# Kernel optimization log

Measured on AMD Instinct MI355X. Metric: run time of the kernel, lower is better.

Reference implementation:

```python
import jax, jax.numpy as jnp
import numpy as np


def setup_inputs() -> dict:
    key = jax.random.key(0)
    k0, k1, k2, k3 = jax.random.split(key, 4)
    B, N, D, C, F = 8192, 784, 64, 10, 2  # batch, input_dim, bond_dim, num_classes, feature_dim
    x = jax.random.uniform(k0, (B, N), dtype=jnp.float32)  # pixel values in [0,1]
    core0 = jax.random.normal(k1, (F, 1, D), dtype=jnp.float32) * 0.1
    base = jnp.broadcast_to(jnp.eye(D, dtype=jnp.float32), (N - 2, F, D, D))
    cores_mid = base + jax.random.normal(k2, (N - 2, F, D, D), dtype=jnp.float32) * 0.01
    core_last = jax.random.normal(k3, (F, D, C), dtype=jnp.float32) * 0.1
    return {"x": x, "core0": core0, "cores_mid": cores_mid, "core_last": core_last}


def reference(x, core0, cores_mid, core_last):
    EPS = 1e-8
    factor = jnp.float32(np.pi / 2.0)
    # FeatureMap: [B, N] -> [B, N, 2] with (cos, sin)
    feats = jnp.stack([jnp.cos(factor * x), jnp.sin(factor * x)], axis=-1)
    # First site: M = v0 @ A0.squeeze(1)  -> [B, D]
    M = jnp.einsum('bf,fd->bd', feats[:, 0, :], core0[:, 0, :])
    # Sequential left->right contraction over middle sites with per-step L2 normalization
    v_mid = jnp.moveaxis(feats[:, 1:-1, :], 1, 0)  # [N-2, B, 2]

    def step(M, inp):
        v, A = inp  # v: [B, 2], A: [2, D, D]
        Mn = jnp.einsum('bi,bf,fij->bj', M, v, A)
        Mn = Mn / (jnp.linalg.norm(Mn, axis=1, keepdims=True) + EPS)
        return Mn, None

    M, _ = jax.lax.scan(step, M, (v_mid, cores_mid))
    # Last site: logits[b,c] = sum_i M[b,i] * (v_N[b,f] A_N[f,i,c])
    logits = jnp.einsum('bi,bf,fic->bc', M, feats[:, -1, :], core_last)
    return logits
```

## Files before the change

kernel.cpp:

```cpp
#include <hip/hip_runtime.h>

typedef __attribute__((ext_vector_type(8))) short s16x8;
typedef __attribute__((ext_vector_type(4))) float f32x4;
typedef __attribute__((ext_vector_type(4))) int i32x4;

#define NMID 782
#define PI_2 1.5707963267948966f
#define EG_STEP_BYTES 16384
#define EG_ELEMS ((size_t)NMID * 8192)
#define XCH_CH 3072
#define XCH_PAR 6144

__device__ __forceinline__ int cvt_pk_bf16(float a, float b) {
  int r;
  asm("v_cvt_pk_bf16_f32 %0, %1, %2" : "=v"(r) : "v"(a), "v"(b));
  return r;
}

__device__ __forceinline__ f32x4 mfma_bf16(i32x4 a, i32x4 b, f32x4 c) {
  return __builtin_amdgcn_mfma_f32_16x16x32_bf16(
      __builtin_bit_cast(s16x8, a), __builtin_bit_cast(s16x8, b), c, 0, 0, 0);
}

__device__ __forceinline__ unsigned short bf16_rne(float v) {
  unsigned u = __float_as_uint(v);
  return (unsigned short)((u + 0x7FFFu + ((u >> 16) & 1)) >> 16);
}

__global__ __launch_bounds__(256) void prep_eg(const float* __restrict__ cm,
                                               unsigned short* __restrict__ eg) {
  const int n = blockIdx.x;
  const float* src = cm + (size_t)n * 8192;
  unsigned short* dst = eg + (size_t)n * 8192;
#pragma unroll
  for (int it = 0; it < 4; ++it) {
    int row = it * 256 + threadIdx.x;
    int q = row >> 6, l = row & 63;
    int t = q >> 2, cc = q & 3;
    int f = cc >> 1, c2 = cc & 1, h = l >> 4;
    int j = 16 * t + (l & 15);
    unsigned short v8[8];
#pragma unroll
    for (int e = 0; e < 8; ++e) {
      int i = 32 * c2 + 16 * (e >> 2) + 4 * h + (e & 3);
      float val = src[(f * 64 + i) * 64 + j] - (i == j ? 1.0f : 0.0f);
      v8[e] = bf16_rne(val);
    }
    *(uint4*)(dst + (size_t)row * 8) = *(const uint4*)v8;
  }
}

#define STEP2G(nc, CUR, NXT, X0v, X1v, RS0, RS1)                            \
  {                                                                         \
    int np = (nc) + 3;                                                      \
    if (np >= NMID) np = NMID - 1;                                          \
    const char* pnxt = base + (size_t)np * EG_STEP_BYTES;                   \
    _Pragma("unroll") for (int q = 0; q < 4; ++q)                           \
        NXT[q] = *(const i32x4*)(pnxt + q * 1024);                          \
    float c0, s0, c1, s1;                                                   \
    __sincosf(PI_2 * (X0v), &s0, &c0);                                      \
    __sincosf(PI_2 * (X1v), &s1, &c1);                                      \
    c0 *= (RS0);                                                            \
    s0 *= (RS0);                                                            \
    c1 *= (RS1);                                                            \
    s1 *= (RS1);                                                            \
    f32x4 z = {0.f, 0.f, 0.f, 0.f};                                         \
    __builtin_amdgcn_s_setprio(1);                                          \
    f32x4 aA0 = mfma_bf16(CUR[0], B0g0, z);                                 \
    aA0 = mfma_bf16(CUR[1], B1g0, aA0);                                     \
    f32x4 aB0 = mfma_bf16(CUR[2], B0g0, z);                                 \
    aB0 = mfma_bf16(CUR[3], B1g0, aB0);                                     \
    f32x4 aA1 = mfma_bf16(CUR[0], B0g1, z);                                 \
    aA1 = mfma_bf16(CUR[1], B1g1, aA1);                                     \
    f32x4 aB1 = mfma_bf16(CUR[2], B0g1, z);                                 \
    aB1 = mfma_bf16(CUR[3], B1g1, aB1);                                     \
    __builtin_amdgcn_s_setprio(0);                                          \
    char* wb = xlds + (((nc) + 1) & 1) * XCH_PAR + h * 768 + bl * 48 +      \
               wv * 8;                                                      \
    float cps0 = c0 + s0;                                                   \
    f32x4 mn0;                                                              \
    _Pragma("unroll") for (int r = 0; r < 4; ++r)                           \
        mn0[r] = cps0 * own0[r] + c0 * aA0[r] + s0 * aB0[r];                \
    own0 = mn0;                                                             \
    int2 w0;                                                                \
    w0.x = cvt_pk_bf16(mn0[0], mn0[1]);                                     \
    w0.y = cvt_pk_bf16(mn0[2], mn0[3]);                                     \
    *(int2*)(wb) = w0;                                                      \
    float cps1 = c1 + s1;                                                   \
    f32x4 mn1;                                                              \
    _Pragma("unroll") for (int r = 0; r < 4; ++r)                           \
        mn1[r] = cps1 * own1[r] + c1 * aA1[r] + s1 * aB1[r];                \
    own1 = mn1;                                                             \
    int2 w1;                                                                \
    w1.x = cvt_pk_bf16(mn1[0], mn1[1]);                                     \
    w1.y = cvt_pk_bf16(mn1[2], mn1[3]);                                     \
    *(int2*)(wb + XCH_CH) = w1;                                             \
    asm volatile("s_waitcnt lgkmcnt(0)" ::: "memory");                      \
    __builtin_amdgcn_s_barrier();                                           \
    __builtin_amdgcn_sched_barrier(0);                                      \
    {                                                                       \
      const char* rb =                                                      \
          xlds + (((nc) + 1) & 1) * XCH_PAR + h * 768 + bl * 48;            \
      B0g0 = *(const i32x4*)(rb);                                           \
      B1g0 = *(const i32x4*)(rb + 16);                                      \
      B0g1 = *(const i32x4*)(rb + XCH_CH);                                  \
      B1g1 = *(const i32x4*)(rb + XCH_CH + 16);                             \
    }                                                                       \
  }

__global__ __launch_bounds__(256, 2) void mps_main(
    const float* __restrict__ x, const float* __restrict__ core0,
    const float* __restrict__ core_last, const unsigned short* __restrict__ eg,
    float* __restrict__ out) {
  __shared__ alignas(16) char xlds[2 * XCH_PAR];
  const int lane = threadIdx.x & 63;
  const int wv = threadIdx.x >> 6;
  const int bl = lane & 15;
  const int h = lane >> 4;
  const int b0 = blockIdx.x * 32 + bl;
  const int b1 = b0 + 16;
  const float* xr0 = x + (size_t)b0 * 784;
  const float* xr1 = x + (size_t)b1 * 784;
  const char* base = (const char*)eg + (size_t)wv * 4096 + (size_t)lane * 16;

  f32x4 own0, own1;
  i32x4 B0g0, B1g0, B0g1, B1g1;
  {
    float s, c;
    __sincosf(PI_2 * xr0[0], &s, &c);
    float fm[16];
#pragma unroll
    for (int t = 0; t < 4; ++t)
#pragma unroll
      for (int r = 0; r < 4; ++r) {
        int j = 16 * t + 4 * h + r;
        fm[t * 4 + r] = c * core0[j] + s * core0[64 + j];
      }
#pragma unroll
    for (int r = 0; r < 4; ++r) own0[r] = fm[wv * 4 + r];
#pragma unroll
    for (int p = 0; p < 4; ++p) {
      B0g0[p] = cvt_pk_bf16(fm[2 * p], fm[2 * p + 1]);
      B1g0[p] = cvt_pk_bf16(fm[8 + 2 * p], fm[8 + 2 * p + 1]);
    }
  }
  {
    float s, c;
    __sincosf(PI_2 * xr1[0], &s, &c);
    float fm[16];
#pragma unroll
    for (int t = 0; t < 4; ++t)
#pragma unroll
      for (int r = 0; r < 4; ++r) {
        int j = 16 * t + 4 * h + r;
        fm[t * 4 + r] = c * core0[j] + s * core0[64 + j];
      }
#pragma unroll
    for (int r = 0; r < 4; ++r) own1[r] = fm[wv * 4 + r];
#pragma unroll
    for (int p = 0; p < 4; ++p) {
      B0g1[p] = cvt_pk_bf16(fm[2 * p], fm[2 * p + 1]);
      B1g1[p] = cvt_pk_bf16(fm[8 + 2 * p], fm[8 + 2 * p + 1]);
    }
  }

  i32x4 frA[4], frB[4], frC[4], frD[4];
#pragma unroll
  for (int q = 0; q < 4; ++q)
    frA[q] = *(const i32x4*)(base + 0 * EG_STEP_BYTES + q * 1024);
#pragma unroll
  for (int q = 0; q < 4; ++q)
    frB[q] = *(const i32x4*)(base + 1 * EG_STEP_BYTES + q * 1024);
#pragma unroll
  for (int q = 0; q < 4; ++q)
    frC[q] = *(const i32x4*)(base + 2 * EG_STEP_BYTES + q * 1024);

  float xq0[12], xq1[12];
  f32x4 xfA0, xfB0, xfA1, xfB1;
  *(f32x4*)&xq0[0] = *(const f32x4*)(xr0 + 0);
  *(f32x4*)&xq0[4] = *(const f32x4*)(xr0 + 4);
  *(f32x4*)&xq0[8] = *(const f32x4*)(xr0 + 8);
  *(f32x4*)&xq1[0] = *(const f32x4*)(xr1 + 0);
  *(f32x4*)&xq1[4] = *(const f32x4*)(xr1 + 4);
  *(f32x4*)&xq1[8] = *(const f32x4*)(xr1 + 8);

  for (int g = 0; g < 97; ++g) {
    if (g > 0) {
#pragma unroll
      for (int i = 0; i < 4; ++i) {
        xq0[i] = xq0[8 + i];
        xq1[i] = xq1[8 + i];
      }
      *(f32x4*)&xq0[4] = xfA0;
      *(f32x4*)&xq0[8] = xfB0;
      *(f32x4*)&xq1[4] = xfA1;
      *(f32x4*)&xq1[8] = xfB1;
    }
    {
      int xo = (g < 96) ? 8 * g + 12 : 780;
      int xo2 = (g < 96) ? 8 * g + 16 : 780;
      xfA0 = *(const f32x4*)(xr0 + xo);
      xfB0 = *(const f32x4*)(xr0 + xo2);
      xfA1 = *(const f32x4*)(xr1 + xo);
      xfB1 = *(const f32x4*)(xr1 + xo2);
    }

    float rs0 = 1.0f, rs1 = 1.0f;
    if ((g & 7) == 0) {
      float ss0 = 0.f, ss1 = 0.f;
#pragma unroll
      for (int p = 0; p < 4; ++p) {
        unsigned u0 = (unsigned)B0g0[p], u1 = (unsigned)B1g0[p];
        float a0 = __uint_as_float(u0 << 16);
        float a1 = __uint_as_float(u0 & 0xFFFF0000u);
        float d0 = __uint_as_float(u1 << 16);
        float d1 = __uint_as_float(u1 & 0xFFFF0000u);
        ss0 += a0 * a0 + a1 * a1 + d0 * d0 + d1 * d1;
        unsigned v0 = (unsigned)B0g1[p], v1 = (unsigned)B1g1[p];
        float e0 = __uint_as_float(v0 << 16);
        float e1 = __uint_as_float(v0 & 0xFFFF0000u);
        float f0 = __uint_as_float(v1 << 16);
        float f1 = __uint_as_float(v1 & 0xFFFF0000u);
        ss1 += e0 * e0 + e1 * e1 + f0 * f0 + f1 * f1;
      }
      ss0 += __shfl_xor(ss0, 16);
      ss0 += __shfl_xor(ss0, 32);
      ss1 += __shfl_xor(ss1, 16);
      ss1 += __shfl_xor(ss1, 32);
      rs0 = rsqrtf(ss0);
      rs1 = rsqrtf(ss1);
    }

    int n0 = 8 * g;
    STEP2G(n0 + 0, frA, frD, xq0[1], xq1[1], rs0, rs1);
    STEP2G(n0 + 1, frB, frA, xq0[2], xq1[2], 1.0f, 1.0f);
    STEP2G(n0 + 2, frC, frB, xq0[3], xq1[3], 1.0f, 1.0f);
    STEP2G(n0 + 3, frD, frC, xq0[4], xq1[4], 1.0f, 1.0f);
    STEP2G(n0 + 4, frA, frD, xq0[5], xq1[5], 1.0f, 1.0f);
    STEP2G(n0 + 5, frB, frA, xq0[6], xq1[6], 1.0f, 1.0f);
    STEP2G(n0 + 6, frC, frB, xq0[7], xq1[7], 1.0f, 1.0f);
    STEP2G(n0 + 7, frD, frC, xq0[8], xq1[8], 1.0f, 1.0f);
  }

  {
#pragma unroll
    for (int i = 0; i < 4; ++i) {
      xq0[i] = xq0[8 + i];
      xq1[i] = xq1[8 + i];
    }
    *(f32x4*)&xq0[4] = xfA0;
    *(f32x4*)&xq1[4] = xfA1;
    STEP2G(776, frA, frD, xq0[1], xq1[1], 1.0f, 1.0f);
    STEP2G(777, frB, frA, xq0[2], xq1[2], 1.0f, 1.0f);
    STEP2G(778, frC, frB, xq0[3], xq1[3], 1.0f, 1.0f);
    STEP2G(779, frD, frC, xq0[4], xq1[4], 1.0f, 1.0f);
    STEP2G(780, frA, frD, xq0[5], xq1[5], 1.0f, 1.0f);
    STEP2G(781, frB, frA, xq0[6], xq1[6], 1.0f, 1.0f);
  }

  asm volatile("s_waitcnt lgkmcnt(0)" ::: "memory");
  __builtin_amdgcn_s_barrier();
  *(f32x4*)(xlds + wv * 1152 + lane * 16) = own0;
  *(f32x4*)(xlds + 4608 + wv * 1152 + lane * 16) = own1;
  asm volatile("s_waitcnt lgkmcnt(0)" ::: "memory");
  __builtin_amdgcn_s_barrier();
  __builtin_amdgcn_sched_barrier(0);

#pragma unroll
  for (int grp = 0; grp < 2; ++grp) {
    float fm[16];
#pragma unroll
    for (int t = 0; t < 4; ++t) {
      f32x4 v = *(const f32x4*)(xlds + grp * 4608 + t * 1152 + lane * 16);
#pragma unroll
      for (int r = 0; r < 4; ++r) fm[t * 4 + r] = v[r];
    }
    float ss = 0.f;
#pragma unroll
    for (int i = 0; i < 16; ++i) ss += fm[i] * fm[i];
    ss += __shfl_xor(ss, 16);
    ss += __shfl_xor(ss, 32);
    float inv = 1.0f / (sqrtf(ss) + 1e-8f);
#pragma unroll
    for (int i = 0; i < 16; ++i) fm[i] *= inv;

    float xv = grp == 0 ? xq0[7] : xq1[7];
    float s, c;
    __sincosf(PI_2 * xv, &s, &c);
    float part[10];
#pragma unroll
    for (int cc = 0; cc < 10; ++cc) part[cc] = 0.f;
#pragma unroll
    for (int t = 0; t < 4; ++t)
#pragma unroll
      for (int r = 0; r < 4; ++r) {
        int i = 16 * t + 4 * h + r;
        float mv = fm[t * 4 + r];
#pragma unroll
        for (int cc = 0; cc < 10; ++cc)
          part[cc] +=
              mv * (c * core_last[i * 10 + cc] + s * core_last[640 + i * 10 + cc]);
      }
#pragma unroll
    for (int cc = 0; cc < 10; ++cc) {
      part[cc] += __shfl_xor(part[cc], 16);
      part[cc] += __shfl_xor(part[cc], 32);
    }
    if (wv == 0 && h == 0) {
      int brow = grp == 0 ? b0 : b1;
#pragma unroll
      for (int cc = 0; cc < 10; ++cc) out[brow * 10 + cc] = part[cc];
    }
  }
}

__global__ __launch_bounds__(64) void mps_slow(const float* __restrict__ x,
                                               const float* __restrict__ core0,
                                               const float* __restrict__ cm,
                                               const float* __restrict__ cl,
                                               float* __restrict__ out) {
  int b = blockIdx.x * 64 + threadIdx.x;
  float m[64], mn[64];
  float s, c;
  __sincosf(PI_2 * x[(size_t)b * 784], &s, &c);
  for (int d = 0; d < 64; ++d) m[d] = c * core0[d] + s * core0[64 + d];
  for (int n = 0; n < NMID; ++n) {
    __sincosf(PI_2 * x[(size_t)b * 784 + n + 1], &s, &c);
    const float* A0 = cm + (size_t)n * 8192;
    const float* A1 = A0 + 4096;
    for (int j = 0; j < 64; ++j) mn[j] = 0.f;
    for (int i = 0; i < 64; ++i) {
      float w0 = c * m[i], w1 = s * m[i];
      for (int j = 0; j < 64; ++j) mn[j] += w0 * A0[i * 64 + j] + w1 * A1[i * 64 + j];
    }
    float ssn = 0.f;
    for (int j = 0; j < 64; ++j) ssn += mn[j] * mn[j];
    float inv = 1.f / (sqrtf(ssn) + 1e-8f);
    for (int j = 0; j < 64; ++j) m[j] = mn[j] * inv;
  }
  __sincosf(PI_2 * x[(size_t)b * 784 + 783], &s, &c);
  for (int cc = 0; cc < 10; ++cc) {
    float acc = 0.f;
    for (int i = 0; i < 64; ++i)
      acc += m[i] * (c * cl[i * 10 + cc] + s * cl[640 + i * 10 + cc]);
    out[b * 10 + cc] = acc;
  }
}

extern "C" void kernel_launch(void* const* d_in, const int* in_sizes, int n_in,
                              void* d_out, int out_size, void* d_ws, size_t ws_size,
                              hipStream_t stream) {
  const float* x = (const float*)d_in[0];
  const float* core0 = (const float*)d_in[1];
  const float* cm = (const float*)d_in[2];
  const float* cl = (const float*)d_in[3];
  float* out = (float*)d_out;
  size_t need = EG_ELEMS * sizeof(unsigned short);
  if (ws_size >= need) {
    unsigned short* eg = (unsigned short*)d_ws;
    prep_eg<<<NMID, 256, 0, stream>>>(cm, eg);
    mps_main<<<256, 256, 0, stream>>>(x, core0, cl, eg, out);
  } else {
    mps_slow<<<8192 / 64, 64, 0, stream>>>(x, core0, cm, cl, out);
  }
}
```

Baseline: 245.9 us.

## Collapse four-wave block into single wave per 32 rows, removing LDS exchange

Each block now uses one 64-lane wavefront that computes all four 16-column output tiles of the 64-wide state itself, instead of splitting them across four waves that exchanged bf16 state through LDS with a barrier every step. This removes the per-step LDS write/read and block barrier. In exchange each wave issues four times the MFMAs per step, holds the whole core slice (16 x 16B fragments, double buffered) in registers with only one step of prefetch, and the grid drops to 256 single-wave blocks, so far fewer waves are available to hide the serial MFMA and load latency.

```diff
diff --git a/kernel.cpp b/kernel.cpp
--- a/kernel.cpp
+++ b/kernel.cpp
@@ -8,8 +8,6 @@
 #define PI_2 1.5707963267948966f
 #define EG_STEP_BYTES 16384
 #define EG_ELEMS ((size_t)NMID * 8192)
-#define XCH_CH 3072
-#define XCH_PAR 6144
 
 __device__ __forceinline__ int cvt_pk_bf16(float a, float b) {
   int r;
@@ -50,12 +48,12 @@
   }
 }
 
-#define STEP2G(nc, CUR, NXT, X0v, X1v, RS0, RS1)                            \
+#define STEP2C(nc, CUR, NXT, X0v, X1v, RS0, RS1)                            \
   {                                                                         \
-    int np = (nc) + 3;                                                      \
+    int np = (nc) + 1;                                                      \
     if (np >= NMID) np = NMID - 1;                                          \
     const char* pnxt = base + (size_t)np * EG_STEP_BYTES;                   \
-    _Pragma("unroll") for (int q = 0; q < 4; ++q)                           \
+    _Pragma("unroll") for (int q = 0; q < 16; ++q)                          \
         NXT[q] = *(const i32x4*)(pnxt + q * 1024);                          \
     float c0, s0, c1, s1;                                                   \
     __sincosf(PI_2 * (X0v), &s0, &c0);                                      \
@@ -64,116 +62,77 @@
     s0 *= (RS0);                                                            \
     c1 *= (RS1);                                                            \
     s1 *= (RS1);                                                            \
+    float cps0 = c0 + s0, cps1 = c1 + s1;                                   \
     f32x4 z = {0.f, 0.f, 0.f, 0.f};                                         \
-    __builtin_amdgcn_s_setprio(1);                                          \
-    f32x4 aA0 = mfma_bf16(CUR[0], B0g0, z);                                 \
-    aA0 = mfma_bf16(CUR[1], B1g0, aA0);                                     \
-    f32x4 aB0 = mfma_bf16(CUR[2], B0g0, z);                                 \
-    aB0 = mfma_bf16(CUR[3], B1g0, aB0);                                     \
-    f32x4 aA1 = mfma_bf16(CUR[0], B0g1, z);                                 \
-    aA1 = mfma_bf16(CUR[1], B1g1, aA1);                                     \
-    f32x4 aB1 = mfma_bf16(CUR[2], B0g1, z);                                 \
-    aB1 = mfma_bf16(CUR[3], B1g1, aB1);                                     \
-    __builtin_amdgcn_s_setprio(0);                                          \
-    char* wb = xlds + (((nc) + 1) & 1) * XCH_PAR + h * 768 + bl * 48 +      \
-               wv * 8;                                                      \
-    float cps0 = c0 + s0;                                                   \
-    f32x4 mn0;                                                              \
-    _Pragma("unroll") for (int r = 0; r < 4; ++r)                           \
-        mn0[r] = cps0 * own0[r] + c0 * aA0[r] + s0 * aB0[r];                \
-    own0 = mn0;                                                             \
-    int2 w0;                                                                \
-    w0.x = cvt_pk_bf16(mn0[0], mn0[1]);                                     \
-    w0.y = cvt_pk_bf16(mn0[2], mn0[3]);                                     \
-    *(int2*)(wb) = w0;                                                      \
-    float cps1 = c1 + s1;                                                   \
-    f32x4 mn1;                                                              \
-    _Pragma("unroll") for (int r = 0; r < 4; ++r)                           \
-        mn1[r] = cps1 * own1[r] + c1 * aA1[r] + s1 * aB1[r];                \
-    own1 = mn1;                                                             \
-    int2 w1;                                                                \
-    w1.x = cvt_pk_bf16(mn1[0], mn1[1]);                                     \
-    w1.y = cvt_pk_bf16(mn1[2], mn1[3]);                                     \
-    *(int2*)(wb + XCH_CH) = w1;                                             \
-    asm volatile("s_waitcnt lgkmcnt(0)" ::: "memory");                      \
-    __builtin_amdgcn_s_barrier();                                           \
-    __builtin_amdgcn_sched_barrier(0);                                      \
-    {                                                                       \
-      const char* rb =                                                      \
-          xlds + (((nc) + 1) & 1) * XCH_PAR + h * 768 + bl * 48;            \
-      B0g0 = *(const i32x4*)(rb);                                           \
-      B1g0 = *(const i32x4*)(rb + 16);                                      \
-      B0g1 = *(const i32x4*)(rb + XCH_CH);                                  \
-      B1g1 = *(const i32x4*)(rb + XCH_CH + 16);                             \
+    _Pragma("unroll") for (int t = 0; t < 4; ++t) {                         \
+      __builtin_amdgcn_s_setprio(1);                                        \
+      f32x4 aA0 = mfma_bf16(CUR[4 * t + 0], B0a, z);                        \
+      aA0 = mfma_bf16(CUR[4 * t + 1], B1a, aA0);                            \
+      f32x4 aB0 = mfma_bf16(CUR[4 * t + 2], B0a, z);                        \
+      aB0 = mfma_bf16(CUR[4 * t + 3], B1a, aB0);                            \
+      f32x4 aA1 = mfma_bf16(CUR[4 * t + 0], B0b, z);                        \
+      aA1 = mfma_bf16(CUR[4 * t + 1], B1b, aA1);                            \
+      f32x4 aB1 = mfma_bf16(CUR[4 * t + 2], B0b, z);                        \
+      aB1 = mfma_bf16(CUR[4 * t + 3], B1b, aB1);                            \
+      __builtin_amdgcn_s_setprio(0);                                        \
+      _Pragma("unroll") for (int r = 0; r < 4; ++r) {                       \
+        m0[4 * t + r] = cps0 * m0[4 * t + r] + c0 * aA0[r] + s0 * aB0[r];   \
+        m1[4 * t + r] = cps1 * m1[4 * t + r] + c1 * aA1[r] + s1 * aB1[r];   \
+      }                                                                     \
     }                                                                       \
-  }
-
-__global__ __launch_bounds__(256, 2) void mps_main(
+    _Pragma("unroll") for (int p = 0; p < 4; ++p) {                         \
+      B0a[p] = cvt_pk_bf16(m0[2 * p], m0[2 * p + 1]);                       \
+      B1a[p] = cvt_pk_bf16(m0[8 + 2 * p], m0[8 + 2 * p + 1]);               \
+      B0b[p] = cvt_pk_bf16(m1[2 * p], m1[2 * p + 1]);                       \
+      B1b[p] = cvt_pk_bf16(m1[8 + 2 * p], m1[8 + 2 * p + 1]);               \
+    }                                                                       \
+  }
+
+__global__ __launch_bounds__(64) void mps_main(
     const float* __restrict__ x, const float* __restrict__ core0,
     const float* __restrict__ core_last, const unsigned short* __restrict__ eg,
     float* __restrict__ out) {
-  __shared__ alignas(16) char xlds[2 * XCH_PAR];
-  const int lane = threadIdx.x & 63;
-  const int wv = threadIdx.x >> 6;
+  const int lane = threadIdx.x;
   const int bl = lane & 15;
   const int h = lane >> 4;
   const int b0 = blockIdx.x * 32 + bl;
   const int b1 = b0 + 16;
   const float* xr0 = x + (size_t)b0 * 784;
   const float* xr1 = x + (size_t)b1 * 784;
-  const char* base = (const char*)eg + (size_t)wv * 4096 + (size_t)lane * 16;
-
-  f32x4 own0, own1;
-  i32x4 B0g0, B1g0, B0g1, B1g1;
+  const char* base = (const char*)eg + (size_t)lane * 16;
+
+  float m0[16], m1[16];
+  i32x4 B0a, B1a, B0b, B1b;
   {
     float s, c;
     __sincosf(PI_2 * xr0[0], &s, &c);
-    float fm[16];
 #pragma unroll
     for (int t = 0; t < 4; ++t)
 #pragma unroll
       for (int r = 0; r < 4; ++r) {
         int j = 16 * t + 4 * h + r;
-        fm[t * 4 + r] = c * core0[j] + s * core0[64 + j];
-      }
-#pragma unroll
-    for (int r = 0; r < 4; ++r) own0[r] = fm[wv * 4 + r];
-#pragma unroll
-    for (int p = 0; p < 4; ++p) {
-      B0g0[p] = cvt_pk_bf16(fm[2 * p], fm[2 * p + 1]);
-      B1g0[p] = cvt_pk_bf16(fm[8 + 2 * p], fm[8 + 2 * p + 1]);
-    }
-  }
-  {
-    float s, c;
+        m0[t * 4 + r] = c * core0[j] + s * core0[64 + j];
+      }
     __sincosf(PI_2 * xr1[0], &s, &c);
-    float fm[16];
 #pragma unroll
     for (int t = 0; t < 4; ++t)
 #pragma unroll
       for (int r = 0; r < 4; ++r) {
         int j = 16 * t + 4 * h + r;
-        fm[t * 4 + r] = c * core0[j] + s * core0[64 + j];
-      }
-#pragma unroll
-    for (int r = 0; r < 4; ++r) own1[r] = fm[wv * 4 + r];
+        m1[t * 4 + r] = c * core0[j] + s * core0[64 + j];
+      }
 #pragma unroll
     for (int p = 0; p < 4; ++p) {
-      B0g1[p] = cvt_pk_bf16(fm[2 * p], fm[2 * p + 1]);
-      B1g1[p] = cvt_pk_bf16(fm[8 + 2 * p], fm[8 + 2 * p + 1]);
-    }
-  }
-
-  i32x4 frA[4], frB[4], frC[4], frD[4];
-#pragma unroll
-  for (int q = 0; q < 4; ++q)
-    frA[q] = *(const i32x4*)(base + 0 * EG_STEP_BYTES + q * 1024);
-#pragma unroll
-  for (int q = 0; q < 4; ++q)
-    frB[q] = *(const i32x4*)(base + 1 * EG_STEP_BYTES + q * 1024);
-#pragma unroll
-  for (int q = 0; q < 4; ++q)
-    frC[q] = *(const i32x4*)(base + 2 * EG_STEP_BYTES + q * 1024);
+      B0a[p] = cvt_pk_bf16(m0[2 * p], m0[2 * p + 1]);
+      B1a[p] = cvt_pk_bf16(m0[8 + 2 * p], m0[8 + 2 * p + 1]);
+      B0b[p] = cvt_pk_bf16(m1[2 * p], m1[2 * p + 1]);
+      B1b[p] = cvt_pk_bf16(m1[8 + 2 * p], m1[8 + 2 * p + 1]);
+    }
+  }
+
+  i32x4 frA[16], frB[16];
+#pragma unroll
+  for (int q = 0; q < 16; ++q) frA[q] = *(const i32x4*)(base + q * 1024);
 
   float xq0[12], xq1[12];
   f32x4 xfA0, xfB0, xfA1, xfB1;
@@ -209,19 +168,9 @@
     if ((g & 7) == 0) {
       float ss0 = 0.f, ss1 = 0.f;
 #pragma unroll
-      for (int p = 0; p < 4; ++p) {
-        unsigned u0 = (unsigned)B0g0[p], u1 = (unsigned)B1g0[p];
-        float a0 = __uint_as_float(u0 << 16);
-        float a1 = __uint_as_float(u0 & 0xFFFF0000u);
-        float d0 = __uint_as_float(u1 << 16);
-        float d1 = __uint_as_float(u1 & 0xFFFF0000u);
-        ss0 += a0 * a0 + a1 * a1 + d0 * d0 + d1 * d1;
-        unsigned v0 = (unsigned)B0g1[p], v1 = (unsigned)B1g1[p];
-        float e0 = __uint_as_float(v0 << 16);
-        float e1 = __uint_as_float(v0 & 0xFFFF0000u);
-        float f0 = __uint_as_float(v1 << 16);
-        float f1 = __uint_as_float(v1 & 0xFFFF0000u);
-        ss1 += e0 * e0 + e1 * e1 + f0 * f0 + f1 * f1;
+      for (int i = 0; i < 16; ++i) {
+        ss0 += m0[i] * m0[i];
+        ss1 += m1[i] * m1[i];
       }
       ss0 += __shfl_xor(ss0, 16);
       ss0 += __shfl_xor(ss0, 32);
@@ -232,14 +181,14 @@
     }
 
     int n0 = 8 * g;
-    STEP2G(n0 + 0, frA, frD, xq0[1], xq1[1], rs0, rs1);
-    STEP2G(n0 + 1, frB, frA, xq0[2], xq1[2], 1.0f, 1.0f);
-    STEP2G(n0 + 2, frC, frB, xq0[3], xq1[3], 1.0f, 1.0f);
-    STEP2G(n0 + 3, frD, frC, xq0[4], xq1[4], 1.0f, 1.0f);
-    STEP2G(n0 + 4, frA, frD, xq0[5], xq1[5], 1.0f, 1.0f);
-    STEP2G(n0 + 5, frB, frA, xq0[6], xq1[6], 1.0f, 1.0f);
-    STEP2G(n0 + 6, frC, frB, xq0[7], xq1[7], 1.0f, 1.0f);
-    STEP2G(n0 + 7, frD, frC, xq0[8], xq1[8], 1.0f, 1.0f);
+    STEP2C(n0 + 0, frA, frB, xq0[1], xq1[1], rs0, rs1);
+    STEP2C(n0 + 1, frB, frA, xq0[2], xq1[2], 1.0f, 1.0f);
+    STEP2C(n0 + 2, frA, frB, xq0[3], xq1[3], 1.0f, 1.0f);
+    STEP2C(n0 + 3, frB, frA, xq0[4], xq1[4], 1.0f, 1.0f);
+    STEP2C(n0 + 4, frA, frB, xq0[5], xq1[5], 1.0f, 1.0f);
+    STEP2C(n0 + 5, frB, frA, xq0[6], xq1[6], 1.0f, 1.0f);
+    STEP2C(n0 + 6, frA, frB, xq0[7], xq1[7], 1.0f, 1.0f);
+    STEP2C(n0 + 7, frB, frA, xq0[8], xq1[8], 1.0f, 1.0f);
   }
 
   {
@@ -250,31 +199,19 @@
     }
     *(f32x4*)&xq0[4] = xfA0;
     *(f32x4*)&xq1[4] = xfA1;
-    STEP2G(776, frA, frD, xq0[1], xq1[1], 1.0f, 1.0f);
-    STEP2G(777, frB, frA, xq0[2], xq1[2], 1.0f, 1.0f);
-    STEP2G(778, frC, frB, xq0[3], xq1[3], 1.0f, 1.0f);
-    STEP2G(779, frD, frC, xq0[4], xq1[4], 1.0f, 1.0f);
-    STEP2G(780, frA, frD, xq0[5], xq1[5], 1.0f, 1.0f);
-    STEP2G(781, frB, frA, xq0[6], xq1[6], 1.0f, 1.0f);
-  }
-
-  asm volatile("s_waitcnt lgkmcnt(0)" ::: "memory");
-  __builtin_amdgcn_s_barrier();
-  *(f32x4*)(xlds + wv * 1152 + lane * 16) = own0;
-  *(f32x4*)(xlds + 4608 + wv * 1152 + lane * 16) = own1;
-  asm volatile("s_waitcnt lgkmcnt(0)" ::: "memory");
-  __builtin_amdgcn_s_barrier();
-  __builtin_amdgcn_sched_barrier(0);
+    STEP2C(776, frA, frB, xq0[1], xq1[1], 1.0f, 1.0f);
+    STEP2C(777, frB, frA, xq0[2], xq1[2], 1.0f, 1.0f);
+    STEP2C(778, frA, frB, xq0[3], xq1[3], 1.0f, 1.0f);
+    STEP2C(779, frB, frA, xq0[4], xq1[4], 1.0f, 1.0f);
+    STEP2C(780, frA, frB, xq0[5], xq1[5], 1.0f, 1.0f);
+    STEP2C(781, frB, frA, xq0[6], xq1[6], 1.0f, 1.0f);
+  }
 
 #pragma unroll
   for (int grp = 0; grp < 2; ++grp) {
     float fm[16];
 #pragma unroll
-    for (int t = 0; t < 4; ++t) {
-      f32x4 v = *(const f32x4*)(xlds + grp * 4608 + t * 1152 + lane * 16);
-#pragma unroll
-      for (int r = 0; r < 4; ++r) fm[t * 4 + r] = v[r];
-    }
+    for (int i = 0; i < 16; ++i) fm[i] = grp == 0 ? m0[i] : m1[i];
     float ss = 0.f;
 #pragma unroll
     for (int i = 0; i < 16; ++i) ss += fm[i] * fm[i];
@@ -306,7 +243,7 @@
       part[cc] += __shfl_xor(part[cc], 16);
       part[cc] += __shfl_xor(part[cc], 32);
     }
-    if (wv == 0 && h == 0) {
+    if (h == 0) {
       int brow = grp == 0 ? b0 : b1;
 #pragma unroll
       for (int cc = 0; cc < 10; ++cc) out[brow * 10 + cc] = part[cc];
@@ -359,7 +296,7 @@
   if (ws_size >= need) {
     unsigned short* eg = (unsigned short*)d_ws;
     prep_eg<<<NMID, 256, 0, stream>>>(cm, eg);
-    mps_main<<<256, 256, 0, stream>>>(x, core0, cl, eg, out);
+    mps_main<<<256, 64, 0, stream>>>(x, core0, cl, eg, out);
   } else {
     mps_slow<<<8192 / 64, 64, 0, stream>>>(x, core0, cm, cl, out);
   }
```

After: 576.2 us. 2.34x slower.
